# Kernel tuning notes

Hardware: AMD Instinct MI355X
Metric: run time of the kernel (lower is better)

The kernel has to match this reference:

```python
import jax, jax.numpy as jnp
import numpy as np

B, L, E, H = 4, 2048, 512, 8
D = E // H
FACTOR = 5
U = min(FACTOR * int(np.ceil(np.log(L))), L)  # sample_k == n_top == 40


def setup_inputs() -> dict:
    key0 = jax.random.key(0)
    ks = jax.random.split(key0, 12)
    s = 0.02
    inp = {
        "query": jax.random.normal(ks[0], (B, L, E), jnp.float32),
        "key": jax.random.normal(ks[1], (B, L, E), jnp.float32),
        "value": jax.random.normal(ks[2], (B, L, E), jnp.float32),
        "index_sample": jax.random.randint(ks[3], (L, U), 0, L, jnp.int32),
    }
    for i, nm in enumerate(["q", "k", "v", "o"]):
        inp[f"W{nm}"] = jax.random.normal(ks[4 + i], (E, E), jnp.float32) * s
        inp[f"b{nm}"] = jnp.zeros((E,), jnp.float32)
    return inp


def reference(query, key, value, index_sample, Wq, bq, Wk, bk, Wv, bv, Wo, bo):
    # projections (nn.Linear: x @ W.T + b)
    q = (query @ Wq.T + bq).reshape(B, L, H, D).transpose(0, 2, 1, 3)  # [B,H,L,D]
    k = (key @ Wk.T + bk).reshape(B, L, H, D).transpose(0, 2, 1, 3)
    v = (value @ Wv.T + bv).reshape(B, L, H, D).transpose(0, 2, 1, 3)

    L_Q = L_K = L
    sample_k = index_sample.shape[1]
    n_top = min(sample_k, L_Q)

    # --- _prob_QK: sampled QK scores, note: NO 1/sqrt(D) scaling in source ---
    K_sample = k[:, :, index_sample, :]                      # [B,H,L_Q,sample_k,D]
    QK_sample = jnp.einsum('bhld,bhlsd->bhls', q, K_sample)  # [B,H,L_Q,sample_k]
    M = QK_sample.max(axis=-1) - QK_sample.sum(axis=-1) / L_K
    _, M_top = jax.lax.top_k(M, n_top)                       # [B,H,n_top]
    Q_reduce = jnp.take_along_axis(q, M_top[..., None], axis=2)  # [B,H,n_top,D]
    scores = jnp.einsum('bhud,bhkd->bhuk', Q_reduce, k)      # [B,H,n_top,L_K]

    # --- initial context (eval mode: mean of V) ---
    context = jnp.broadcast_to(v.mean(axis=2, keepdims=True), (B, H, L_Q, D))

    # --- update context at selected queries ---
    attn = jax.nn.softmax(scores, axis=-1)
    upd = jnp.einsum('bhuk,bhkd->bhud', attn, v)             # [B,H,n_top,D]
    bi = jnp.arange(B)[:, None, None]
    hi = jnp.arange(H)[None, :, None]
    context = context.at[bi, hi, M_top].set(upd)

    out = context.transpose(0, 2, 1, 3).reshape(B, L, E) @ Wo.T + bo
    return out
```

## Files before the change

### kernel.cpp

```cpp
#include <hip/hip_runtime.h>
#include <hip/hip_bf16.h>
#include <math.h>

constexpr int BB = 4;
constexpr int LL = 2048;
constexpr int EE = 512;
constexpr int HH = 8;
constexpr int DD = 64;
constexpr int UU = 40;
constexpr int NT = 40;
constexpr int NCH = 32;
constexpr int CK = 64;
constexpr int MVC = 16;
constexpr float NEG_INF = -3.0e38f;

typedef __attribute__((ext_vector_type(8))) short bf8_t;
typedef __attribute__((ext_vector_type(4))) float f4_t;

__device__ __forceinline__ void split2pair(float x0, float x1, uint& hp, uint& mp)
{
    uint xb0 = __float_as_uint(x0), xb1 = __float_as_uint(x1);
    uint hb0 = xb0 + 0x7fffu + ((xb0 >> 16) & 1u);
    uint hb1 = xb1 + 0x7fffu + ((xb1 >> 16) & 1u);
    hp = __builtin_amdgcn_perm(hb1, hb0, 0x07060302u);
    float r0 = x0 - __uint_as_float(hb0 & 0xffff0000u);
    float r1 = x1 - __uint_as_float(hb1 & 0xffff0000u);
    mp = __builtin_amdgcn_perm(__float_as_uint(r1), __float_as_uint(r0), 0x07060302u);
}

__device__ __forceinline__ void gload16(const void* g, void* l)
{
    __builtin_amdgcn_global_load_lds(
        (const __attribute__((address_space(1))) unsigned int*)g,
        (__attribute__((address_space(3))) unsigned int*)l, 16, 0, 0);
}

__device__ __forceinline__ int swz(int row, int c)
{
    return row * 64 + (((c ^ row ^ (row >> 2)) & 3) << 4);
}

__global__ __launch_bounds__(256) void wconv_kernel(
    const float* __restrict__ Wq, const float* __restrict__ Wk,
    const float* __restrict__ Wv, unsigned short* __restrict__ wcv)
{
    const int gi  = blockIdx.x * 256 + threadIdx.x;
    const int z   = gi >> 15;
    const int off = (gi & 32767) * 8;
    const float* W = (z == 0) ? Wq : (z == 1 ? Wk : Wv);
    float x[8];
    *(float4*)(x)     = *(const float4*)(W + off);
    *(float4*)(x + 4) = *(const float4*)(W + off + 4);
    uint hp[4], mp[4];
#pragma unroll
    for (int p = 0; p < 4; p++) split2pair(x[2 * p], x[2 * p + 1], hp[p], mp[p]);
    unsigned short* Wh = wcv + (size_t)z * 524288;
    *(uint4*)(Wh + off)          = make_uint4(hp[0], hp[1], hp[2], hp[3]);
    *(uint4*)(Wh + 262144 + off) = make_uint4(mp[0], mp[1], mp[2], mp[3]);
}

__global__ __launch_bounds__(256, 3) void proj_kernel(
    const float* __restrict__ Xq, const float* __restrict__ Xk, const float* __restrict__ Xv,
    const unsigned short* __restrict__ Wcv,
    const float* __restrict__ bq, const float* __restrict__ bk, const float* __restrict__ bv,
    float* __restrict__ Oq, float* __restrict__ Ok, float* __restrict__ Ov)
{
    const int bid = blockIdx.x;
    const int xg  = bid & 7;
    const int s   = bid >> 3;
    const int yz  = xg * 24 + (s >> 2);
    const int zi  = yz >> 6;
    const int yi  = yz & 63;
    const int m0  = yi * 128;
    const int n0  = (s & 3) * 128;

    const float* X; const float* bias; float* O;
    if (zi == 0)      { X = Xq; bias = bq; O = Oq; }
    else if (zi == 1) { X = Xk; bias = bk; O = Ok; }
    else              { X = Xv; bias = bv; O = Ov; }
    const unsigned short* Wh = Wcv + (size_t)zi * 524288;
    const unsigned short* Wm = Wh + 262144;

    __shared__ char ldsmem[49152];
    char* const LA = ldsmem;
    char* const LB = ldsmem + 16384;

    const int tid  = threadIdx.x;
    const int lane = tid & 63;
    const int wave = tid >> 6;

    const int srow  = tid >> 1;
    const int shalf = tid & 1;
    const int w0 = swz(srow, shalf * 2);
    const int w1 = swz(srow, shalf * 2 + 1);
    const float* Aptr = X + (size_t)(m0 + srow) * EE + shalf * 16;

    const int r0 = tid >> 2;
    const int r1 = 64 + r0;
    const int c0 = (tid & 3) ^ ((r0 ^ (r0 >> 2)) & 3);
    const int c1 = (tid & 3) ^ ((r1 ^ (r1 >> 2)) & 3);
    const unsigned short* bh0 = Wh + (size_t)(n0 + r0) * EE + c0 * 8;
    const unsigned short* bh1 = Wh + (size_t)(n0 + r1) * EE + c1 * 8;
    const unsigned short* bm0 = Wm + (size_t)(n0 + r0) * EE + c0 * 8;
    const unsigned short* bm1 = Wm + (size_t)(n0 + r1) * EE + c1 * 8;
    const int ldst = tid * 16;

    const int rxor = ((((lane >> 4) ^ lane ^ (lane >> 2)) & 3) << 4);
    const int arow = (wave >> 1) * 64 + (lane & 15);
    const int brow = (wave & 1) * 64 + (lane & 15);

    f4_t acc[4][4];
#pragma unroll
    for (int i = 0; i < 4; i++)
#pragma unroll
        for (int j = 0; j < 4; j++) acc[i][j] = (f4_t)0.0f;

    float fa[16];
#pragma unroll
    for (int q = 0; q < 4; q++)
        *(float4*)(fa + q * 4) = *(const float4*)(Aptr + q * 4);
    gload16(bh0, LB + ldst);
    gload16(bh1, LB + 4096 + ldst);
    gload16(bm0, LB + 8192 + ldst);
    gload16(bm1, LB + 12288 + ldst);

    int parity = 0;
#pragma unroll 2
    for (int kt = 0; kt < EE; kt += 32) {
        uint ahu[8], amu[8];
#pragma unroll
        for (int p = 0; p < 8; p++)
            split2pair(fa[2 * p], fa[2 * p + 1], ahu[p], amu[p]);

        __syncthreads();
        *(uint4*)(LA +    0 + w0) = make_uint4(ahu[0], ahu[1], ahu[2], ahu[3]);
        *(uint4*)(LA +    0 + w1) = make_uint4(ahu[4], ahu[5], ahu[6], ahu[7]);
        *(uint4*)(LA + 8192 + w0) = make_uint4(amu[0], amu[1], amu[2], amu[3]);
        *(uint4*)(LA + 8192 + w1) = make_uint4(amu[4], amu[5], amu[6], amu[7]);
        __syncthreads();

        if (kt + 32 < EE) {
            const int kn = kt + 32;
#pragma unroll
            for (int q = 0; q < 4; q++)
                *(float4*)(fa + q * 4) = *(const float4*)(Aptr + kn + q * 4);
            char* Bn = LB + (parity ^ 1) * 16384;
            gload16(bh0 + kn, Bn + ldst);
            gload16(bh1 + kn, Bn + 4096 + ldst);
            gload16(bm0 + kn, Bn + 8192 + ldst);
            gload16(bm1 + kn, Bn + 12288 + ldst);
        }

        char* const Bb = LB + parity * 16384;
        bf8_t af[4][2];
#pragma unroll
        for (int i = 0; i < 4; i++) {
            const int ro = (arow + i * 16) * 64 + rxor;
            af[i][0] = *(const bf8_t*)(LA +    0 + ro);
            af[i][1] = *(const bf8_t*)(LA + 8192 + ro);
        }
#pragma unroll
        for (int j = 0; j < 4; j++) {
            const int ro = (brow + j * 16) * 64 + rxor;
            bf8_t bh_ = *(const bf8_t*)(Bb +    0 + ro);
            bf8_t bm_ = *(const bf8_t*)(Bb + 8192 + ro);
#pragma unroll
            for (int i = 0; i < 4; i++) {
                f4_t c = acc[i][j];
                c = __builtin_amdgcn_mfma_f32_16x16x32_bf16(af[i][0], bh_, c, 0, 0, 0);
                c = __builtin_amdgcn_mfma_f32_16x16x32_bf16(af[i][0], bm_, c, 0, 0, 0);
                c = __builtin_amdgcn_mfma_f32_16x16x32_bf16(af[i][1], bh_, c, 0, 0, 0);
                acc[i][j] = c;
            }
        }
        parity ^= 1;
    }

#pragma unroll
    for (int j = 0; j < 4; j++) {
        const int n  = n0 + (wave & 1) * 64 + j * 16 + (lane & 15);
        const float bn = bias[n];
        const int h_ = n >> 6, d_ = n & 63;
#pragma unroll
        for (int i = 0; i < 4; i++) {
            const int mb = m0 + (wave >> 1) * 64 + i * 16 + ((lane >> 4) << 2);
#pragma unroll
            for (int r = 0; r < 4; r++) {
                const int m  = mb + r;
                const int b_ = m >> 11;
                const int l_ = m & (LL - 1);
                O[(((size_t)(b_ * HH + h_) * LL + l_) << 6) + d_] = acc[i][j][r] + bn;
            }
        }
    }
}

__global__ __launch_bounds__(256) void meanv_part_kernel(const float* __restrict__ v,
                                                         float* __restrict__ vpart)
{
    const int bh    = blockIdx.x & 31;
    const int chunk = blockIdx.x >> 5;
    const int d  = threadIdx.x & 63;
    const int wv = threadIdx.x >> 6;
    const float* base = v + ((size_t)bh * LL + chunk * 128 + wv * 32) * DD + d;
    float acc = 0.0f;
#pragma unroll
    for (int i = 0; i < 32; i++) acc += base[i * DD];
    __shared__ float red[4][DD];
    red[wv][d] = acc;
    __syncthreads();
    if (wv == 0)
        vpart[(size_t)(chunk * 32 + bh) * DD + d]
            = red[0][d] + red[1][d] + red[2][d] + red[3][d];
}

__global__ __launch_bounds__(64) void meanv_comb_kernel(const float* __restrict__ vpart,
                                                        float* __restrict__ mean_v)
{
    const int bh = blockIdx.x;
    const int d  = threadIdx.x;
    float s = 0.0f;
#pragma unroll
    for (int c = 0; c < MVC; c++) s += vpart[(size_t)(c * 32 + bh) * DD + d];
    mean_v[bh * DD + d] = s * (1.0f / (float)LL);
}

__global__ __launch_bounds__(256) void measure_kernel(const float* __restrict__ q,
                                                      const float* __restrict__ k,
                                                      const int* __restrict__ idx_sample,
                                                      float* __restrict__ M)
{
    int bh   = blockIdx.x & 31;
    int lc   = blockIdx.x >> 5;
    int lane = threadIdx.x & 63;
    int wv   = threadIdx.x >> 6;
    int l    = lc * 4 + wv;
    int s8   = lane >> 3;
    int c    = lane & 7;

    const float* qrow = q + ((size_t)bh * LL + l) * DD + c * 8;
    float4 q0 = *(const float4*)(qrow);
    float4 q1 = *(const float4*)(qrow + 4);

    const float* kbase = k + (size_t)bh * LL * DD;
    const int*   irow  = idx_sample + l * UU;

    float mx = NEG_INF, sum = 0.0f;
#pragma unroll
    for (int it = 0; it < UU; it += 8) {
        int ki = irow[it + s8];
        const float* krow = kbase + (size_t)ki * DD + c * 8;
        float4 k0 = *(const float4*)(krow);
        float4 k1 = *(const float4*)(krow + 4);
        float p = q0.x*k0.x + q0.y*k0.y + q0.z*k0.z + q0.w*k0.w
                + q1.x*k1.x + q1.y*k1.y + q1.z*k1.z + q1.w*k1.w;
        p += __shfl_xor(p, 1, 64);
        p += __shfl_xor(p, 2, 64);
        p += __shfl_xor(p, 4, 64);
        mx = fmaxf(mx, p);
        sum += p;
    }
    mx  = fmaxf(mx, __shfl_xor(mx, 8, 64));
    sum += __shfl_xor(sum, 8, 64);
    mx  = fmaxf(mx, __shfl_xor(mx, 16, 64));
    sum += __shfl_xor(sum, 16, 64);
    mx  = fmaxf(mx, __shfl_xor(mx, 32, 64));
    sum += __shfl_xor(sum, 32, 64);

    if (lane == 0) M[bh * LL + l] = mx - sum * (1.0f / (float)LL);
}

__global__ __launch_bounds__(64) void topk_kernel(const float* __restrict__ M,
                                                  int* __restrict__ top)
{
    const int bh   = blockIdx.x;
    const int lane = threadIdx.x;

    unsigned long long keys[32];
#pragma unroll
    for (int i = 0; i < 32; i++) {
        int idx = i * 64 + lane;
        uint u  = __float_as_uint(M[bh * LL + idx]);
        uint sv = (u & 0x80000000u) ? ~u : (u | 0x80000000u);
        keys[i] = ((unsigned long long)sv << 32) | (uint)(LL - 1 - idx);
    }
    unsigned long long lmax = 0ull;
#pragma unroll
    for (int i = 0; i < 32; i++) lmax = (keys[i] > lmax) ? keys[i] : lmax;

    for (int it = 0; it < NT; it++) {
        unsigned long long g = lmax;
#pragma unroll
        for (int off = 1; off < 64; off <<= 1) {
            unsigned long long o = __shfl_xor(g, off, 64);
            g = (o > g) ? o : g;
        }
        if (lane == 0) top[bh * NT + it] = LL - 1 - (int)(g & 0xffffffffu);
#pragma unroll
        for (int i = 0; i < 32; i++) if (keys[i] == g) keys[i] = 0ull;
        lmax = 0ull;
#pragma unroll
        for (int i = 0; i < 32; i++) lmax = (keys[i] > lmax) ? keys[i] : lmax;
    }
}

__global__ __launch_bounds__(256) void pv_kernel(const float* __restrict__ q,
                                                 const float* __restrict__ k,
                                                 const float* __restrict__ v,
                                                 const int* __restrict__ top,
                                                 float* __restrict__ mpart,
                                                 float* __restrict__ lpart,
                                                 float* __restrict__ accpart)
{
    const int bh    = blockIdx.x & 31;
    const int chunk = blockIdx.x >> 5;
    const int tid   = threadIdx.x;
    const int lane  = tid & 63, wv = tid >> 6;

    __shared__ float qs[NT][DD];
    __shared__ float sc[NT][CK + 4];

    for (int i = tid; i < NT * DD / 4; i += 256) {
        int u  = i >> 4;
        int d4 = (i & 15) * 4;
        int l  = top[bh * NT + u];
        *(float4*)&qs[u][d4] = *(const float4*)(q + ((size_t)bh * LL + l) * DD + d4);
    }
    __syncthreads();

    {
        const int key  = tid >> 2;
        const int dseg = tid & 3;
        const float* krow = k + ((size_t)bh * LL + chunk * CK + key) * DD + dseg * 16;
        float4 k0 = *(const float4*)(krow);
        float4 k1 = *(const float4*)(krow + 4);
        float4 k2 = *(const float4*)(krow + 8);
        float4 k3 = *(const float4*)(krow + 12);
#pragma unroll 8
        for (int u = 0; u < NT; u++) {
            const float* qrow = &qs[u][dseg * 16];
            float4 q0 = *(const float4*)(qrow);
            float4 q1 = *(const float4*)(qrow + 4);
            float4 q2 = *(const float4*)(qrow + 8);
            float4 q3 = *(const float4*)(qrow + 12);
            float p = k0.x*q0.x + k0.y*q0.y + k0.z*q0.z + k0.w*q0.w
                    + k1.x*q1.x + k1.y*q1.y + k1.z*q1.z + k1.w*q1.w
                    + k2.x*q2.x + k2.y*q2.y + k2.z*q2.z + k2.w*q2.w
                    + k3.x*q3.x + k3.y*q3.y + k3.z*q3.z + k3.w*q3.w;
            p += __shfl_xor(p, 1, 64);
            p += __shfl_xor(p, 2, 64);
            if (dseg == 0) sc[u][key] = p;
        }
    }
    __syncthreads();

#pragma unroll
    for (int i = 0; i < 10; i++) {
        const int u = wv * 10 + i;
        float val = sc[u][lane];
        float mx = val;
        mx = fmaxf(mx, __shfl_xor(mx, 1, 64));
        mx = fmaxf(mx, __shfl_xor(mx, 2, 64));
        mx = fmaxf(mx, __shfl_xor(mx, 4, 64));
        mx = fmaxf(mx, __shfl_xor(mx, 8, 64));
        mx = fmaxf(mx, __shfl_xor(mx, 16, 64));
        mx = fmaxf(mx, __shfl_xor(mx, 32, 64));
        float e = __expf(val - mx);
        sc[u][lane] = e;
        float s = e;
        s += __shfl_xor(s, 1, 64);
        s += __shfl_xor(s, 2, 64);
        s += __shfl_xor(s, 4, 64);
        s += __shfl_xor(s, 8, 64);
        s += __shfl_xor(s, 16, 64);
        s += __shfl_xor(s, 32, 64);
        if (lane == 0) {
            mpart[(bh * NCH + chunk) * NT + u] = mx;
            lpart[(bh * NCH + chunk) * NT + u] = s;
        }
    }
    __syncthreads();

    {
        float pacc[10];
#pragma unroll
        for (int i = 0; i < 10; i++) pacc[i] = 0.0f;
        const float* vbase = v + ((size_t)bh * LL + chunk * CK) * DD;
#pragma unroll 8
        for (int t = 0; t < CK; t++) {
            float vval = vbase[(size_t)t * DD + lane];
#pragma unroll
            for (int i = 0; i < 10; i++) pacc[i] += sc[wv * 10 + i][t] * vval;
        }
#pragma unroll
        for (int i = 0; i < 10; i++) {
            const int u = wv * 10 + i;
            accpart[(((size_t)(bh * NCH + chunk)) * NT + u) * 64 + lane] = pacc[i];
        }
    }
}

__global__ __launch_bounds__(256) void base_kernel(const float* __restrict__ mean_v,
                                                   const float* __restrict__ Wo,
                                                   const float* __restrict__ bo,
                                                   float* __restrict__ base)
{
    int lane = threadIdx.x & 63, wv = threadIdx.x >> 6;
    int be = blockIdx.x * 4 + wv;
    int b  = be >> 9;
    int e  = be & (EE - 1);
    const float* mrow = mean_v + b * EE;
    const float* wrow = Wo + (size_t)e * EE;
    float acc = 0.0f;
#pragma unroll
    for (int j = 0; j < 8; j++) acc += mrow[lane + j * 64] * wrow[lane + j * 64];
#pragma unroll
    for (int off = 32; off > 0; off >>= 1) acc += __shfl_down(acc, off, 64);
    if (lane == 0) base[be] = acc + bo[e];
}

__global__ __launch_bounds__(256) void bcast_kernel(const float* __restrict__ base,
                                                    float* __restrict__ out)
{
    size_t fi = ((size_t)blockIdx.x * 256 + threadIdx.x) * 4;
    int b  = (int)(fi >> 20);
    int e4 = (int)(fi & (EE - 1));
    float4 val = *(const float4*)(base + b * EE + e4);
    *(float4*)(out + fi) = val;
}

__global__ __launch_bounds__(64) void delta_kernel(const float* __restrict__ accpart,
                                                   const float* __restrict__ lpart,
                                                   const float* __restrict__ mpart,
                                                   const float* __restrict__ mean_v,
                                                   float* __restrict__ delta_ws)
{
    const int bhu = blockIdx.x;
    const int bh  = bhu / NT;
    const int u   = bhu % NT;
    const int d   = threadIdx.x;

    const float* mp = mpart + (size_t)bh * NCH * NT + u;
    const float* lp = lpart + (size_t)bh * NCH * NT + u;
    const float* ap = accpart + ((size_t)bh * NCH * NT + u) * 64 + d;

    float m = NEG_INF;
#pragma unroll
    for (int c = 0; c < NCH; c++) m = fmaxf(m, mp[c * NT]);
    float den = 0.0f, num = 0.0f;
#pragma unroll
    for (int c = 0; c < NCH; c++) {
        float f = __expf(mp[c * NT] - m);
        den += lp[c * NT] * f;
        num += ap[(size_t)c * NT * 64] * f;
    }
    delta_ws[(size_t)bhu * 64 + d] = num / den - mean_v[bh * DD + d];
}

__global__ __launch_bounds__(256) void corr2_kernel(const float* __restrict__ delta_ws,
                                                    const int* __restrict__ top,
                                                    const float* __restrict__ Wo,
                                                    float* __restrict__ out)
{
    const int bh  = blockIdx.x & 31;
    const int ec  = blockIdx.x >> 5;
    const int h   = bh & (HH - 1);
    const int b   = bh >> 3;
    const int tid = threadIdx.x;
    const int lane = tid & 63;
    const int wv   = tid >> 6;

    __shared__ alignas(16) float dl[NT][DD];
    __shared__ int ltab[NT];

    for (int i = tid; i < NT * DD / 4; i += 256) {
        const int u  = i >> 4;
        const int d4 = (i & 15) * 4;
        *(float4*)&dl[u][d4] = *(const float4*)(delta_ws + ((size_t)(bh * NT + u)) * 64 + d4);
    }
    if (tid < NT) ltab[tid] = top[bh * NT + tid];

    const int e = ec * 64 + lane;
    const float* wrow = Wo + (size_t)e * EE + h * DD;
    float4 wo[16];
#pragma unroll
    for (int j = 0; j < 16; j++) wo[j] = *(const float4*)(wrow + j * 4);

    __syncthreads();

    float* obase = out + (size_t)b * LL * EE + e;
#pragma unroll
    for (int uu = 0; uu < 10; uu++) {
        const int u = wv * 10 + uu;
        float acc = 0.0f;
#pragma unroll
        for (int j = 0; j < 16; j++) {
            float4 dv = *(const float4*)&dl[u][j * 4];
            acc = fmaf(dv.x, wo[j].x, acc);
            acc = fmaf(dv.y, wo[j].y, acc);
            acc = fmaf(dv.z, wo[j].z, acc);
            acc = fmaf(dv.w, wo[j].w, acc);
        }
        atomicAdd(obase + (size_t)ltab[u] * EE, acc);
    }
}

extern "C" void kernel_launch(void* const* d_in, const int* in_sizes, int n_in,
                              void* d_out, int out_size, void* d_ws, size_t ws_size,
                              hipStream_t stream)
{
    const float* query = (const float*)d_in[0];
    const float* key   = (const float*)d_in[1];
    const float* value = (const float*)d_in[2];
    const int*   idxs  = (const int*)d_in[3];
    const float* Wq = (const float*)d_in[4];
    const float* bq = (const float*)d_in[5];
    const float* Wk = (const float*)d_in[6];
    const float* bk = (const float*)d_in[7];
    const float* Wv = (const float*)d_in[8];
    const float* bv = (const float*)d_in[9];
    const float* Wo = (const float*)d_in[10];
    const float* bo = (const float*)d_in[11];
    float* out = (float*)d_out;

    char* ws = (char*)d_ws;
    size_t off = 0;
    const size_t qkv_bytes = (size_t)BB * HH * LL * DD * sizeof(float);
    float* q_ws = (float*)(ws + off); off += qkv_bytes;
    float* k_ws = (float*)(ws + off); off += qkv_bytes;
    float* v_ws = (float*)(ws + off); off += qkv_bytes;
    float* M_ws    = (float*)(ws + off); off += (size_t)BB * HH * LL * sizeof(float);
    int*   top_ws  = (int*)(ws + off);   off += (size_t)BB * HH * NT * sizeof(int);
    float* mean_ws = (float*)(ws + off); off += (size_t)BB * HH * DD * sizeof(float);
    float* vpart_ws = (float*)(ws + off); off += (size_t)BB * HH * MVC * DD * sizeof(float);
    float* mpart_ws = (float*)(ws + off); off += (size_t)BB * HH * NCH * NT * sizeof(float);
    float* lpart_ws = (float*)(ws + off); off += (size_t)BB * HH * NCH * NT * sizeof(float);
    float* accpart_ws = (float*)(ws + off); off += (size_t)BB * HH * NCH * NT * DD * sizeof(float);
    float* base_ws = (float*)(ws + off); off += (size_t)BB * EE * sizeof(float);
    float* delta_ws = (float*)(ws + off); off += (size_t)BB * HH * NT * DD * sizeof(float);

    unsigned short* wcv_ws = (unsigned short*)accpart_ws;

    wconv_kernel<<<384, 256, 0, stream>>>(Wq, Wk, Wv, wcv_ws);
    proj_kernel<<<768, 256, 0, stream>>>(query, key, value, wcv_ws, bq, bk, bv,
                                         q_ws, k_ws, v_ws);
    meanv_part_kernel<<<BB * HH * MVC, 256, 0, stream>>>(v_ws, vpart_ws);
    meanv_comb_kernel<<<BB * HH, 64, 0, stream>>>(vpart_ws, mean_ws);
    measure_kernel<<<(LL / 4) * 32, 256, 0, stream>>>(q_ws, k_ws, idxs, M_ws);
    topk_kernel<<<BB * HH, 64, 0, stream>>>(M_ws, top_ws);
    pv_kernel<<<BB * HH * NCH, 256, 0, stream>>>(q_ws, k_ws, v_ws, top_ws,
                                                 mpart_ws, lpart_ws, accpart_ws);
    base_kernel<<<(BB * EE) / 4, 256, 0, stream>>>(mean_ws, Wo, bo, base_ws);
    bcast_kernel<<<(BB * LL * EE) / (256 * 4), 256, 0, stream>>>(base_ws, out);
    delta_kernel<<<BB * HH * NT, 64, 0, stream>>>(accpart_ws, lpart_ws, mpart_ws,
                                                  mean_ws, delta_ws);
    corr2_kernel<<<256, 256, 0, stream>>>(delta_ws, top_ws, Wo, out);
}
```

Before: 272.0 us.

## Keep PV scores in registers, broadcast via readlane, and remap blocks by head group

The PV stage no longer writes the exponentials back to shared memory and rereads them per key. Each wave now keeps its raw scores in registers, recomputes the exponentials against per-row maxima held in LDS, and broadcasts them with readlane against 16 V rows it has preloaded. The four waves' partial sums are then reduced through LDS. The block index is also remapped so that neighbouring blocks share head groups, likely for cache locality. This adds register pressure from the 40-entry score array plus 16 V registers, and adds an extra reduction pass through LDS.

```diff
diff --git a/kernel.cpp b/kernel.cpp
--- a/kernel.cpp
+++ b/kernel.cpp
@@ -40,6 +40,11 @@
     return row * 64 + (((c ^ row ^ (row >> 2)) & 3) << 4);
 }
 
+__device__ __forceinline__ float rdlane(float x, int l)
+{
+    return __uint_as_float(__builtin_amdgcn_readlane(__float_as_uint(x), l));
+}
+
 __global__ __launch_bounds__(256) void wconv_kernel(
     const float* __restrict__ Wq, const float* __restrict__ Wk,
     const float* __restrict__ Wv, unsigned short* __restrict__ wcv)
@@ -230,8 +235,10 @@
                                                       const int* __restrict__ idx_sample,
                                                       float* __restrict__ M)
 {
-    int bh   = blockIdx.x & 31;
-    int lc   = blockIdx.x >> 5;
+    const int xg = blockIdx.x & 7;
+    const int sb = blockIdx.x >> 3;
+    const int bh = xg * 4 + (sb & 3);
+    const int lc = sb >> 2;
     int lane = threadIdx.x & 63;
     int wv   = threadIdx.x >> 6;
     int l    = lc * 4 + wv;
@@ -312,13 +319,18 @@
                                                  float* __restrict__ lpart,
                                                  float* __restrict__ accpart)
 {
-    const int bh    = blockIdx.x & 31;
-    const int chunk = blockIdx.x >> 5;
+    const int xg    = blockIdx.x & 7;
+    const int sb    = blockIdx.x >> 3;
+    const int bh    = xg * 4 + (sb & 3);
+    const int chunk = sb >> 2;
     const int tid   = threadIdx.x;
     const int lane  = tid & 63, wv = tid >> 6;
 
-    __shared__ float qs[NT][DD];
-    __shared__ float sc[NT][CK + 4];
+    __shared__ alignas(16) char plds[41120];
+    float (*qs)[DD]     = (float (*)[DD])(plds);
+    float (*sc)[CK + 4] = (float (*)[CK + 4])(plds + 10240);
+    float* red          = (float*)(plds);
+    float* mxs          = (float*)(plds + 40960);
 
     for (int i = tid; i < NT * DD / 4; i += 256) {
         int u  = i >> 4;
@@ -328,6 +340,7 @@
     }
     __syncthreads();
 
+    float p[NT];
     {
         const int key  = tid >> 2;
         const int dseg = tid & 3;
@@ -336,20 +349,21 @@
         float4 k1 = *(const float4*)(krow + 4);
         float4 k2 = *(const float4*)(krow + 8);
         float4 k3 = *(const float4*)(krow + 12);
-#pragma unroll 8
+#pragma unroll
         for (int u = 0; u < NT; u++) {
             const float* qrow = &qs[u][dseg * 16];
             float4 q0 = *(const float4*)(qrow);
             float4 q1 = *(const float4*)(qrow + 4);
             float4 q2 = *(const float4*)(qrow + 8);
             float4 q3 = *(const float4*)(qrow + 12);
-            float p = k0.x*q0.x + k0.y*q0.y + k0.z*q0.z + k0.w*q0.w
-                    + k1.x*q1.x + k1.y*q1.y + k1.z*q1.z + k1.w*q1.w
-                    + k2.x*q2.x + k2.y*q2.y + k2.z*q2.z + k2.w*q2.w
-                    + k3.x*q3.x + k3.y*q3.y + k3.z*q3.z + k3.w*q3.w;
-            p += __shfl_xor(p, 1, 64);
-            p += __shfl_xor(p, 2, 64);
-            if (dseg == 0) sc[u][key] = p;
+            float pp = k0.x*q0.x + k0.y*q0.y + k0.z*q0.z + k0.w*q0.w
+                     + k1.x*q1.x + k1.y*q1.y + k1.z*q1.z + k1.w*q1.w
+                     + k2.x*q2.x + k2.y*q2.y + k2.z*q2.z + k2.w*q2.w
+                     + k3.x*q3.x + k3.y*q3.y + k3.z*q3.z + k3.w*q3.w;
+            pp += __shfl_xor(pp, 1, 64);
+            pp += __shfl_xor(pp, 2, 64);
+            p[u] = pp;
+            if (dseg == 0) sc[u][key] = pp;
         }
     }
     __syncthreads();
@@ -366,7 +380,6 @@
         mx = fmaxf(mx, __shfl_xor(mx, 16, 64));
         mx = fmaxf(mx, __shfl_xor(mx, 32, 64));
         float e = __expf(val - mx);
-        sc[u][lane] = e;
         float s = e;
         s += __shfl_xor(s, 1, 64);
         s += __shfl_xor(s, 2, 64);
@@ -377,26 +390,50 @@
         if (lane == 0) {
             mpart[(bh * NCH + chunk) * NT + u] = mx;
             lpart[(bh * NCH + chunk) * NT + u] = s;
+            mxs[u] = mx;
         }
     }
     __syncthreads();
 
     {
-        float pacc[10];
-#pragma unroll
-        for (int i = 0; i < 10; i++) pacc[i] = 0.0f;
-        const float* vbase = v + ((size_t)bh * LL + chunk * CK) * DD;
-#pragma unroll 8
-        for (int t = 0; t < CK; t++) {
-            float vval = vbase[(size_t)t * DD + lane];
-#pragma unroll
-            for (int i = 0; i < 10; i++) pacc[i] += sc[wv * 10 + i][t] * vval;
-        }
-#pragma unroll
-        for (int i = 0; i < 10; i++) {
-            const int u = wv * 10 + i;
-            accpart[(((size_t)(bh * NCH + chunk)) * NT + u) * 64 + lane] = pacc[i];
-        }
+        float vr[16];
+        const float* vbase = v + ((size_t)bh * LL + chunk * CK + wv * 16) * DD + lane;
+#pragma unroll
+        for (int j = 0; j < 16; j++) vr[j] = vbase[(size_t)j * DD];
+
+#pragma unroll
+        for (int ug = 0; ug < 10; ug++) {
+            float4 mx4 = *(const float4*)&mxs[ug * 4];
+            float e0 = __expf(p[ug * 4 + 0] - mx4.x);
+            float e1 = __expf(p[ug * 4 + 1] - mx4.y);
+            float e2 = __expf(p[ug * 4 + 2] - mx4.z);
+            float e3 = __expf(p[ug * 4 + 3] - mx4.w);
+            float a0 = 0.0f, a1 = 0.0f, a2 = 0.0f, a3 = 0.0f;
+#pragma unroll
+            for (int j = 0; j < 16; j++) {
+                const float vv = vr[j];
+                a0 = fmaf(rdlane(e0, 4 * j), vv, a0);
+                a1 = fmaf(rdlane(e1, 4 * j), vv, a1);
+                a2 = fmaf(rdlane(e2, 4 * j), vv, a2);
+                a3 = fmaf(rdlane(e3, 4 * j), vv, a3);
+            }
+            red[(wv * NT + ug * 4 + 0) * 64 + lane] = a0;
+            red[(wv * NT + ug * 4 + 1) * 64 + lane] = a1;
+            red[(wv * NT + ug * 4 + 2) * 64 + lane] = a2;
+            red[(wv * NT + ug * 4 + 3) * 64 + lane] = a3;
+        }
+    }
+    __syncthreads();
+
+#pragma unroll
+    for (int i = 0; i < 10; i++) {
+        const int u = wv * 10 + i;
+        float s0 = red[(0 * NT + u) * 64 + lane];
+        float s1 = red[(1 * NT + u) * 64 + lane];
+        float s2 = red[(2 * NT + u) * 64 + lane];
+        float s3 = red[(3 * NT + u) * 64 + lane];
+        accpart[(((size_t)(bh * NCH + chunk)) * NT + u) * 64 + lane]
+            = ((s0 + s1) + s2) + s3;
     }
 }
 
```

New measurement: 282.6 us. 1.04x slower.
